# Optimization experiments

Measured on AMD Instinct MI355X. Metric: run time of the kernel, lower is better.

Reference implementation:

```python
import jax, jax.numpy as jnp
import numpy as np

B, D, K = 32768, 256, 4096
BETA = 0.25

def setup_inputs() -> dict:
    key = jax.random.key(0)
    k1, k2 = jax.random.split(key)
    z_e = jax.random.normal(k1, (B, D), dtype=jnp.float32)
    # matches nn.Embedding init: uniform(-1/K, 1/K)
    codebook_weight = jax.random.uniform(k2, (K, D), dtype=jnp.float32,
                                         minval=-1.0 / K, maxval=1.0 / K)
    return {"z_e": z_e, "codebook_weight": codebook_weight}

def reference(z_e, codebook_weight):
    # squared L2 distances [B, K] via expansion: ||z||^2 + ||w||^2 - 2 z.w
    distances = (jnp.sum(z_e ** 2, axis=1, keepdims=True)
                 + jnp.sum(codebook_weight ** 2, axis=1)
                 - 2.0 * z_e @ codebook_weight.T)
    indices = jnp.argmin(distances, axis=1)            # [B] int
    z_q = codebook_weight[indices]                     # [B, D] gather

    codebook_loss = jnp.mean((z_q - jax.lax.stop_gradient(z_e)) ** 2)
    commitment_loss = jnp.mean((z_e - jax.lax.stop_gradient(z_q)) ** 2)
    quant_loss = codebook_loss + BETA * commitment_loss

    # straight-through estimator
    z_q_st = z_e + jax.lax.stop_gradient(z_q - z_e)

    # perplexity: avoid materializing [B, K] one-hot; bincount == one_hot.mean
    counts = jnp.bincount(indices, length=K).astype(jnp.float32)
    avg_probs = counts / z_e.shape[0]
    perplexity = jnp.exp(-jnp.sum(avg_probs * jnp.log(avg_probs + 1e-10)))

    return z_q_st, indices, quant_loss, perplexity
```

## Files before the change

kernel.cpp:

```cpp
#include <hip/hip_runtime.h>
#include <math.h>

constexpr int NROWS = 32768;
constexpr int DIMC  = 256;
constexpr int KC    = 4096;

typedef __attribute__((ext_vector_type(8))) short short8;
typedef __attribute__((ext_vector_type(4))) float f32x4;

#define AS1 __attribute__((address_space(1)))
#define AS3 __attribute__((address_space(3)))

#define WINQ 420u

__device__ __forceinline__ unsigned short f2bf(float x) {
  unsigned u = __float_as_uint(x);
  return (unsigned short)((u + 0x7fffu + ((u >> 16) & 1u)) >> 16);
}

__global__ __launch_bounds__(256)
void vq_prep(const float* __restrict__ Z, const float* __restrict__ W,
             unsigned short* __restrict__ Zh, unsigned short* __restrict__ Wh) {
  const bool isW = blockIdx.x >= 1024;
  const int bid  = isW ? ((int)blockIdx.x - 1024) : (int)blockIdx.x;
  const float* X = isW ? W : Z;
  unsigned short* out = isW ? Wh : Zh;
  const int blk = bid >> 2;
  const int kb0 = (bid & 3) * 2;
  const int t = threadIdx.x;

#pragma unroll
  for (int kk = 0; kk < 2; ++kk) {
    const int kb = kb0 + kk;
#pragma unroll
    for (int gi = 0; gi < 2; ++gi) {
      const int g = t + gi * 256;
      const int r = g >> 2, slot = g & 3;
      const int s8 = slot ^ ((r >> 1) & 3);
      const float* src = X + (size_t)(blk * 128 + r) * DIMC + kb * 32 + s8 * 8;
      short8 vh;
#pragma unroll
      for (int j = 0; j < 8; ++j) vh[j] = (short)f2bf(src[j]);
      *(short8*)(out + ((size_t)blk * 8 + kb) * 4096 + g * 8) = vh;
    }
  }
}

#define DPP_MIN4(v)                                                            \
  {                                                                            \
    unsigned _t;                                                               \
    _t = (unsigned)__builtin_amdgcn_update_dpp((int)(v), (int)(v), 0x121, 0xF, 0xF, false); \
    (v) = min((v), _t);                                                        \
    _t = (unsigned)__builtin_amdgcn_update_dpp((int)(v), (int)(v), 0x122, 0xF, 0xF, false); \
    (v) = min((v), _t);                                                        \
    _t = (unsigned)__builtin_amdgcn_update_dpp((int)(v), (int)(v), 0x124, 0xF, 0xF, false); \
    (v) = min((v), _t);                                                        \
    _t = (unsigned)__builtin_amdgcn_update_dpp((int)(v), (int)(v), 0x128, 0xF, 0xF, false); \
    (v) = min((v), _t);                                                        \
  }

__global__ __launch_bounds__(256, 4)
void vq_mfma(const unsigned short* __restrict__ Zh, const unsigned short* __restrict__ Wh,
             uint2* __restrict__ partial) {
  __shared__ char lds[16384];
  const int t = threadIdx.x, lane = t & 63, w = t >> 6;
  const int rb = blockIdx.x >> 5, cb = blockIdx.x & 31;
  const int q = lane >> 4, ml = lane & 15;
  const int wr = w >> 1, wc = w & 1;

  const unsigned short* bsrc = Wh + (size_t)cb * 32768 + (w >> 1) * 4096
                             + (w & 1) * 2048 + lane * 8;
  char* bdst = lds + (w >> 1) * 8192 + (w & 1) * 4096;

  int aoff[4], boff[4];
#pragma unroll
  for (int i = 0; i < 4; ++i) {
    const int r = wr * 64 + i * 16 + ml;
    aoff[i] = (r * 4 + (q ^ ((r >> 1) & 3))) * 16;
    const int c = wc * 64 + i * 16 + ml;
    boff[i] = (c * 4 + (q ^ ((c >> 1) & 3))) * 16;
  }
  const char* Abase = (const char*)Zh + (size_t)rb * 65536;

  f32x4 acc[4][4];
#pragma unroll
  for (int i = 0; i < 4; ++i)
#pragma unroll
    for (int j = 0; j < 4; ++j) acc[i][j] = (f32x4){0.f, 0.f, 0.f, 0.f};

  for (int kb2 = 0; kb2 < 4; ++kb2) {
    __syncthreads();
#pragma unroll
    for (int i = 0; i < 4; ++i)
      __builtin_amdgcn_global_load_lds((const AS1 void*)(bsrc + kb2 * 8192 + i * 512),
                                       (AS3 void*)(bdst + i * 1024), 16, 0, 0);
    short8 Af[2][4];
#pragma unroll
    for (int sec = 0; sec < 2; ++sec) {
      const int kb = kb2 * 2 + sec;
#pragma unroll
      for (int i = 0; i < 4; ++i)
        Af[sec][i] = *(const short8*)(Abase + (size_t)kb * 8192 + aoff[i]);
    }
    __syncthreads();
#pragma unroll
    for (int sec = 0; sec < 2; ++sec) {
      short8 Bf[4];
#pragma unroll
      for (int i = 0; i < 4; ++i)
        Bf[i] = *(const short8*)(lds + sec * 8192 + boff[i]);
#pragma unroll
      for (int i = 0; i < 4; ++i)
#pragma unroll
        for (int j = 0; j < 4; ++j)
          acc[i][j] = __builtin_amdgcn_mfma_f32_16x16x32_bf16(Af[sec][i], Bf[j], acc[i][j], 0, 0, 0);
    }
  }

  __syncthreads();
  uint2* pk = (uint2*)lds;
  const float SCN = -4194304.0f;

#pragma unroll
  for (int i = 0; i < 4; ++i) {
#pragma unroll
    for (int r = 0; r < 4; ++r) {
      unsigned k[4];
#pragma unroll
      for (int j = 0; j < 4; ++j) {
        const unsigned qv = (unsigned)fmaf(acc[i][j][r], SCN, 524288.0f);
        k[j] = (qv << 7) + (unsigned)(wc * 64 + j * 16 + ml);
      }
      const unsigned m01 = min(k[0], k[1]), x01 = max(k[0], k[1]);
      const unsigned m23 = min(k[2], k[3]), x23 = max(k[2], k[3]);
      const unsigned k1l = min(m01, m23);
      const unsigned k2l = min(max(m01, m23), min(x01, x23));
      unsigned m1 = k1l;
      DPP_MIN4(m1)
      unsigned c2 = (k1l == m1) ? k2l : k1l;
      DPP_MIN4(c2)
      if (ml == 0) pk[w * 64 + (i * 16 + q * 4 + r)] = make_uint2(m1, c2);
    }
  }
  __syncthreads();
  if (t < 128) {
    const int wrh = t >> 6, lr = t & 63;
    const uint2 A2 = pk[(wrh * 2 + 0) * 64 + lr];
    const uint2 B2 = pk[(wrh * 2 + 1) * 64 + lr];
    const unsigned k1 = min(A2.x, B2.x);
    const unsigned k2 = min(min(A2.y, B2.y), max(A2.x, B2.x));
    const unsigned g1 = ((k1 >> 7) << 12) | ((unsigned)cb << 7) | (k1 & 127u);
    const unsigned g2 = ((k2 >> 7) << 12) | ((unsigned)cb << 7) | (k2 & 127u);
    const int row = rb * 128 + wrh * 64 + lr;
    partial[(size_t)row * 32 + cb] = make_uint2(g1, g2);
  }
}

__device__ __forceinline__ float exact_d(const float* __restrict__ Z,
                                         const float* __restrict__ W,
                                         int row, int c, float a) {
  const float* z = Z + (size_t)row * DIMC;
  const float* w = W + (size_t)c * DIMC;
  float dot = 0.f;
  for (int d0 = 0; d0 < DIMC; d0 += 4) {
    const float4 zv = *(const float4*)(z + d0);
    const float4 wv = *(const float4*)(w + d0);
    dot = fmaf(zv.x, wv.x, dot);
    dot = fmaf(zv.y, wv.y, dot);
    dot = fmaf(zv.z, wv.z, dot);
    dot = fmaf(zv.w, wv.w, dot);
  }
  return a - 2.0f * dot;
}

__global__ __launch_bounds__(256)
void vq_tailA(const float* __restrict__ Z, const float* __restrict__ W,
              const uint2* __restrict__ partial, int* __restrict__ kbuf) {
  const int lane = threadIdx.x & 63, wv = threadIdx.x >> 6;
  const int row = blockIdx.x * 4 + wv;
  const float INF = 3.4e38f;

  unsigned k1 = 0xFFFFFFFFu, k2 = 0xFFFFFFFFu;
  if (lane < 32) {
    const uint2 p = partial[(size_t)row * 32 + lane];
    k1 = p.x; k2 = p.y;
  }
  unsigned g1 = k1, g2 = k2;
#pragma unroll
  for (int mask = 1; mask < 32; mask <<= 1) {
    const unsigned og1 = (unsigned)__shfl_xor((int)g1, mask);
    const unsigned og2 = (unsigned)__shfl_xor((int)g2, mask);
    const unsigned mx = max(g1, og1);
    g1 = min(g1, og1);
    g2 = min(min(g2, og2), mx);
  }
  g1 = (unsigned)__shfl((int)g1, 0);
  g2 = (unsigned)__shfl((int)g2, 0);

  int k;
  const unsigned q1 = g1 >> 12;
  if ((g2 >> 12) - q1 > WINQ) {
    k = (int)(g1 & 4095u);
  } else {
    const float4 z4 = *(const float4*)(Z + (size_t)row * DIMC + lane * 4);
    double ns = (double)z4.x * z4.x + (double)z4.y * z4.y +
                (double)z4.z * z4.z + (double)z4.w * z4.w;
#pragma unroll
    for (int mask = 1; mask < 64; mask <<= 1) ns += __shfl_xor(ns, mask);
    const float a = (float)ns;

    const bool scan   = (lane < 32) && ((k2 >> 12) <= q1 + WINQ);
    const bool single = (lane < 32) && !scan && ((k1 >> 12) <= q1 + WINQ);
    float bd = INF; int bi = 0x7fffffff;
    if (single) {
      const int c = (int)(k1 & 4095u);
      const float d = exact_d(Z, W, row, c, a);
      if (d < bd || (d == bd && c < bi)) { bd = d; bi = c; }
    }
    unsigned long long msk = __ballot(scan);
    while (msk) {
      const int cbk = __ffsll(msk) - 1; msk &= msk - 1;
#pragma unroll
      for (int h = 0; h < 2; ++h) {
        const int c = cbk * 128 + h * 64 + lane;
        const float d = exact_d(Z, W, row, c, a);
        if (d < bd || (d == bd && c < bi)) { bd = d; bi = c; }
      }
    }
#pragma unroll
    for (int mask = 1; mask < 64; mask <<= 1) {
      const float od = __shfl_xor(bd, mask);
      const int   oi = __shfl_xor(bi, mask);
      if (od < bd || (od == bd && oi < bi)) { bd = od; bi = oi; }
    }
    k = bi;
  }
  if (lane == 0) kbuf[row] = k;
}

__global__ __launch_bounds__(256)
void vq_tailB(const float* __restrict__ Z, const float* __restrict__ W,
              const int* __restrict__ kbuf, float* __restrict__ zq_out,
              float* __restrict__ idx_out, double* __restrict__ lossp,
              int* __restrict__ hist) {
  __shared__ double sh[4];
  const int lane = threadIdx.x & 63, wv = threadIdx.x >> 6;
  const int row = blockIdx.x * 4 + wv;

  const int k = kbuf[row];
  const float4 z4 = *(const float4*)(Z + (size_t)row * DIMC + lane * 4);
  const float4 w4 = *(const float4*)(W + (size_t)k   * DIMC + lane * 4);
  *(float4*)(zq_out + (size_t)row * DIMC + lane * 4) = w4;

  const double dx = (double)w4.x - (double)z4.x;
  const double dy = (double)w4.y - (double)z4.y;
  const double dz = (double)w4.z - (double)z4.z;
  const double dw = (double)w4.w - (double)z4.w;
  double l = dx * dx + dy * dy + dz * dz + dw * dw;
#pragma unroll
  for (int off = 32; off > 0; off >>= 1) l += __shfl_down(l, off);

  if (lane == 0) { sh[wv] = l; idx_out[row] = (float)k; atomicAdd(&hist[k], 1); }
  __syncthreads();
  if (threadIdx.x == 0) lossp[blockIdx.x] = sh[0] + sh[1] + sh[2] + sh[3];
}

__global__ __launch_bounds__(1024)
void vq_final(const double* __restrict__ lossp, const int* __restrict__ hist,
              float* __restrict__ scal) {
  __shared__ double sL[16], sH[16];
  const int t = threadIdx.x, lane = t & 63, wv = t >> 6;
  double L = 0.0, H = 0.0;
  for (int i = t; i < NROWS / 4; i += 1024) L += lossp[i];
  for (int k = t; k < KC; k += 1024) {
    const double p = (double)hist[k] / (double)NROWS;
    H -= p * log(p + 1e-10);
  }
#pragma unroll
  for (int off = 32; off > 0; off >>= 1) {
    L += __shfl_down(L, off);
    H += __shfl_down(H, off);
  }
  if (lane == 0) { sL[wv] = L; sH[wv] = H; }
  __syncthreads();
  if (t == 0) {
    double LT = 0.0, HT = 0.0;
#pragma unroll
    for (int i = 0; i < 16; ++i) { LT += sL[i]; HT += sH[i]; }
    scal[0] = (float)(LT * 1.25 / ((double)NROWS * (double)DIMC));
    scal[1] = (float)exp(HT);
  }
}

extern "C" void kernel_launch(void* const* d_in, const int* in_sizes, int n_in,
                              void* d_out, int out_size, void* d_ws, size_t ws_size,
                              hipStream_t stream) {
  const float* Z = (const float*)d_in[0];
  const float* W = (const float*)d_in[1];
  float* out = (float*)d_out;
  float* zq_out  = out;
  float* idx_out = out + (size_t)NROWS * DIMC;
  float* scal    = idx_out + NROWS;

  char* ws = (char*)d_ws;
  int*    hist       = (int*)(ws + 1024);
  int*    kbuf       = (int*)(ws + 262144);
  double* lossp      = (double*)(ws + 524288);
  uint2*  partial    = (uint2*)(ws + 1048576);
  unsigned short* Zh = (unsigned short*)(ws + 20971520);
  unsigned short* Wh = (unsigned short*)(ws + 37748736);

  hipMemsetAsync(ws, 0, 17408, stream);
  vq_prep<<<1152, 256, 0, stream>>>(Z, W, Zh, Wh);
  vq_mfma<<<8192, 256, 0, stream>>>(Zh, Wh, partial);
  vq_tailA<<<NROWS / 4, 256, 0, stream>>>(Z, W, partial, kbuf);
  vq_tailB<<<NROWS / 4, 256, 0, stream>>>(Z, W, kbuf, zq_out, idx_out, lossp, hist);
  vq_final<<<1, 1024, 0, stream>>>(lossp, hist, scal);
}
```

Before: 230.1 us.

## Load codebook fragments directly from global into registers with double buffering

Drops the LDS staging of codebook tiles (global_load_lds plus two barriers per step). Each wave now loads its A and B fragments straight from global memory into registers, prefetching the next k-block while the MFMAs for the current one run. The aim is to remove the barrier stalls and LDS traffic. In exchange it doubles fragment register use, which forces launch bounds down from 4 to 3 waves per SIMD, and B tiles are now re-read from global or L2 by each wave instead of being shared through LDS.

```diff
diff --git a/kernel.cpp b/kernel.cpp
--- a/kernel.cpp
+++ b/kernel.cpp
@@ -7,9 +7,6 @@
 
 typedef __attribute__((ext_vector_type(8))) short short8;
 typedef __attribute__((ext_vector_type(4))) float f32x4;
-
-#define AS1 __attribute__((address_space(1)))
-#define AS3 __attribute__((address_space(3)))
 
 #define WINQ 420u
 
@@ -59,18 +56,14 @@
     (v) = min((v), _t);                                                        \
   }
 
-__global__ __launch_bounds__(256, 4)
+__global__ __launch_bounds__(256, 3)
 void vq_mfma(const unsigned short* __restrict__ Zh, const unsigned short* __restrict__ Wh,
              uint2* __restrict__ partial) {
-  __shared__ char lds[16384];
+  __shared__ uint2 pk[256];
   const int t = threadIdx.x, lane = t & 63, w = t >> 6;
   const int rb = blockIdx.x >> 5, cb = blockIdx.x & 31;
   const int q = lane >> 4, ml = lane & 15;
   const int wr = w >> 1, wc = w & 1;
-
-  const unsigned short* bsrc = Wh + (size_t)cb * 32768 + (w >> 1) * 4096
-                             + (w & 1) * 2048 + lane * 8;
-  char* bdst = lds + (w >> 1) * 8192 + (w & 1) * 4096;
 
   int aoff[4], boff[4];
 #pragma unroll
@@ -81,6 +74,7 @@
     boff[i] = (c * 4 + (q ^ ((c >> 1) & 3))) * 16;
   }
   const char* Abase = (const char*)Zh + (size_t)rb * 65536;
+  const char* Bbase = (const char*)Wh + (size_t)cb * 65536;
 
   f32x4 acc[4][4];
 #pragma unroll
@@ -88,37 +82,29 @@
 #pragma unroll
     for (int j = 0; j < 4; ++j) acc[i][j] = (f32x4){0.f, 0.f, 0.f, 0.f};
 
-  for (int kb2 = 0; kb2 < 4; ++kb2) {
-    __syncthreads();
+  short8 Af[2][4], Bf[2][4];
+#pragma unroll
+  for (int i = 0; i < 4; ++i) {
+    Af[0][i] = *(const short8*)(Abase + aoff[i]);
+    Bf[0][i] = *(const short8*)(Bbase + boff[i]);
+  }
+#pragma unroll
+  for (int kb = 0; kb < 8; ++kb) {
+    const int cur = kb & 1, nxt = cur ^ 1;
+    if (kb < 7) {
+#pragma unroll
+      for (int i = 0; i < 4; ++i) {
+        Af[nxt][i] = *(const short8*)(Abase + (kb + 1) * 8192 + aoff[i]);
+        Bf[nxt][i] = *(const short8*)(Bbase + (kb + 1) * 8192 + boff[i]);
+      }
+    }
 #pragma unroll
     for (int i = 0; i < 4; ++i)
-      __builtin_amdgcn_global_load_lds((const AS1 void*)(bsrc + kb2 * 8192 + i * 512),
-                                       (AS3 void*)(bdst + i * 1024), 16, 0, 0);
-    short8 Af[2][4];
-#pragma unroll
-    for (int sec = 0; sec < 2; ++sec) {
-      const int kb = kb2 * 2 + sec;
-#pragma unroll
-      for (int i = 0; i < 4; ++i)
-        Af[sec][i] = *(const short8*)(Abase + (size_t)kb * 8192 + aoff[i]);
-    }
-    __syncthreads();
-#pragma unroll
-    for (int sec = 0; sec < 2; ++sec) {
-      short8 Bf[4];
-#pragma unroll
-      for (int i = 0; i < 4; ++i)
-        Bf[i] = *(const short8*)(lds + sec * 8192 + boff[i]);
-#pragma unroll
-      for (int i = 0; i < 4; ++i)
-#pragma unroll
-        for (int j = 0; j < 4; ++j)
-          acc[i][j] = __builtin_amdgcn_mfma_f32_16x16x32_bf16(Af[sec][i], Bf[j], acc[i][j], 0, 0, 0);
-    }
-  }
-
-  __syncthreads();
-  uint2* pk = (uint2*)lds;
+#pragma unroll
+      for (int j = 0; j < 4; ++j)
+        acc[i][j] = __builtin_amdgcn_mfma_f32_16x16x32_bf16(Af[cur][i], Bf[cur][j], acc[i][j], 0, 0, 0);
+  }
+
   const float SCN = -4194304.0f;
 
 #pragma unroll
```

Result: slower. 265.7 us (+15.4%).

## Fuse tail kernels with last-block reduction and fold memset into prep

Applied to the files above, without the earlier changes.

Merges the argmin refinement, gather/loss/histogram and final reduction kernels into one tail kernel, where the last block to finish (found through an atomic counter) computes the loss and perplexity. Zeroing of the counter and histogram moves from a separate memset into block 0 of the prep kernel. The MFMA kernel's block index is also remapped so that consecutive blocks spread across row and column tiles, which changes cache locality. This removes three launches and the kbuf round trip, at the cost of a serialized single-block final reduction and a dependency on fence and atomic ordering.

```diff
diff --git a/kernel.cpp b/kernel.cpp
--- a/kernel.cpp
+++ b/kernel.cpp
@@ -20,14 +20,22 @@
 
 __global__ __launch_bounds__(256)
 void vq_prep(const float* __restrict__ Z, const float* __restrict__ W,
-             unsigned short* __restrict__ Zh, unsigned short* __restrict__ Wh) {
+             unsigned short* __restrict__ Zh, unsigned short* __restrict__ Wh,
+             int* __restrict__ clr) {
+  const int t = threadIdx.x;
+  if (blockIdx.x == 0) {
+#pragma unroll
+    for (int i = 0; i < 17; ++i) {
+      const int idx = t + i * 256;
+      if (idx < 4352) clr[idx] = 0;
+    }
+  }
   const bool isW = blockIdx.x >= 1024;
   const int bid  = isW ? ((int)blockIdx.x - 1024) : (int)blockIdx.x;
   const float* X = isW ? W : Z;
   unsigned short* out = isW ? Wh : Zh;
   const int blk = bid >> 2;
   const int kb0 = (bid & 3) * 2;
-  const int t = threadIdx.x;
 
 #pragma unroll
   for (int kk = 0; kk < 2; ++kk) {
@@ -64,7 +72,9 @@
              uint2* __restrict__ partial) {
   __shared__ char lds[16384];
   const int t = threadIdx.x, lane = t & 63, w = t >> 6;
-  const int rb = blockIdx.x >> 5, cb = blockIdx.x & 31;
+  const int bid = (int)blockIdx.x;
+  const int sbid = ((bid & 7) << 10) + (bid >> 3);
+  const int rb = sbid >> 5, cb = sbid & 31;
   const int q = lane >> 4, ml = lane & 15;
   const int wr = w >> 1, wc = w & 1;
 
@@ -174,8 +184,13 @@
 }
 
 __global__ __launch_bounds__(256)
-void vq_tailA(const float* __restrict__ Z, const float* __restrict__ W,
-              const uint2* __restrict__ partial, int* __restrict__ kbuf) {
+void vq_tail(const float* __restrict__ Z, const float* __restrict__ W,
+             const uint2* __restrict__ partial, float* __restrict__ zq_out,
+             float* __restrict__ idx_out, double* __restrict__ lossp,
+             int* __restrict__ hist, int* __restrict__ cnt,
+             float* __restrict__ scal) {
+  __shared__ double sh[4];
+  __shared__ int s_last;
   const int lane = threadIdx.x & 63, wv = threadIdx.x >> 6;
   const int row = blockIdx.x * 4 + wv;
   const float INF = 3.4e38f;
@@ -197,12 +212,13 @@
   g1 = (unsigned)__shfl((int)g1, 0);
   g2 = (unsigned)__shfl((int)g2, 0);
 
+  const float4 z4 = *(const float4*)(Z + (size_t)row * DIMC + lane * 4);
+
   int k;
   const unsigned q1 = g1 >> 12;
   if ((g2 >> 12) - q1 > WINQ) {
     k = (int)(g1 & 4095u);
   } else {
-    const float4 z4 = *(const float4*)(Z + (size_t)row * DIMC + lane * 4);
     double ns = (double)z4.x * z4.x + (double)z4.y * z4.y +
                 (double)z4.z * z4.z + (double)z4.w * z4.w;
 #pragma unroll
@@ -235,21 +251,8 @@
     }
     k = bi;
   }
-  if (lane == 0) kbuf[row] = k;
-}
-
-__global__ __launch_bounds__(256)
-void vq_tailB(const float* __restrict__ Z, const float* __restrict__ W,
-              const int* __restrict__ kbuf, float* __restrict__ zq_out,
-              float* __restrict__ idx_out, double* __restrict__ lossp,
-              int* __restrict__ hist) {
-  __shared__ double sh[4];
-  const int lane = threadIdx.x & 63, wv = threadIdx.x >> 6;
-  const int row = blockIdx.x * 4 + wv;
-
-  const int k = kbuf[row];
-  const float4 z4 = *(const float4*)(Z + (size_t)row * DIMC + lane * 4);
-  const float4 w4 = *(const float4*)(W + (size_t)k   * DIMC + lane * 4);
+
+  const float4 w4 = *(const float4*)(W + (size_t)k * DIMC + lane * 4);
   *(float4*)(zq_out + (size_t)row * DIMC + lane * 4) = w4;
 
   const double dx = (double)w4.x - (double)z4.x;
@@ -262,18 +265,26 @@
 
   if (lane == 0) { sh[wv] = l; idx_out[row] = (float)k; atomicAdd(&hist[k], 1); }
   __syncthreads();
-  if (threadIdx.x == 0) lossp[blockIdx.x] = sh[0] + sh[1] + sh[2] + sh[3];
-}
-
-__global__ __launch_bounds__(1024)
-void vq_final(const double* __restrict__ lossp, const int* __restrict__ hist,
-              float* __restrict__ scal) {
-  __shared__ double sL[16], sH[16];
-  const int t = threadIdx.x, lane = t & 63, wv = t >> 6;
+  if (threadIdx.x == 0) {
+    lossp[blockIdx.x] = sh[0] + sh[1] + sh[2] + sh[3];
+    __threadfence();
+    s_last = (atomicAdd(cnt, 1) == (int)gridDim.x - 1) ? 1 : 0;
+  }
+  __syncthreads();
+  if (!s_last) return;
+
+  __shared__ double sL[4], sH[4];
   double L = 0.0, H = 0.0;
-  for (int i = t; i < NROWS / 4; i += 1024) L += lossp[i];
-  for (int k = t; k < KC; k += 1024) {
-    const double p = (double)hist[k] / (double)NROWS;
+  for (int i = threadIdx.x; i < NROWS / 4; i += 256) {
+    const unsigned long long u =
+        __hip_atomic_load((const unsigned long long*)&lossp[i],
+                          __ATOMIC_RELAXED, __HIP_MEMORY_SCOPE_AGENT);
+    L += __longlong_as_double((long long)u);
+  }
+  for (int i = threadIdx.x; i < KC; i += 256) {
+    const int h = __hip_atomic_load(&hist[i], __ATOMIC_RELAXED,
+                                    __HIP_MEMORY_SCOPE_AGENT);
+    const double p = (double)h / (double)NROWS;
     H -= p * log(p + 1e-10);
   }
 #pragma unroll
@@ -283,10 +294,9 @@
   }
   if (lane == 0) { sL[wv] = L; sH[wv] = H; }
   __syncthreads();
-  if (t == 0) {
-    double LT = 0.0, HT = 0.0;
-#pragma unroll
-    for (int i = 0; i < 16; ++i) { LT += sL[i]; HT += sH[i]; }
+  if (threadIdx.x == 0) {
+    const double LT = sL[0] + sL[1] + sL[2] + sL[3];
+    const double HT = sH[0] + sH[1] + sH[2] + sH[3];
     scal[0] = (float)(LT * 1.25 / ((double)NROWS * (double)DIMC));
     scal[1] = (float)exp(HT);
   }
@@ -303,17 +313,15 @@
   float* scal    = idx_out + NROWS;
 
   char* ws = (char*)d_ws;
+  int*    cnt        = (int*)ws;
   int*    hist       = (int*)(ws + 1024);
-  int*    kbuf       = (int*)(ws + 262144);
   double* lossp      = (double*)(ws + 524288);
   uint2*  partial    = (uint2*)(ws + 1048576);
   unsigned short* Zh = (unsigned short*)(ws + 20971520);
   unsigned short* Wh = (unsigned short*)(ws + 37748736);
 
-  hipMemsetAsync(ws, 0, 17408, stream);
-  vq_prep<<<1152, 256, 0, stream>>>(Z, W, Zh, Wh);
+  vq_prep<<<1152, 256, 0, stream>>>(Z, W, Zh, Wh, (int*)ws);
   vq_mfma<<<8192, 256, 0, stream>>>(Zh, Wh, partial);
-  vq_tailA<<<NROWS / 4, 256, 0, stream>>>(Z, W, partial, kbuf);
-  vq_tailB<<<NROWS / 4, 256, 0, stream>>>(Z, W, kbuf, zq_out, idx_out, lossp, hist);
-  vq_final<<<1, 1024, 0, stream>>>(lossp, hist, scal);
-}
+  vq_tail<<<NROWS / 4, 256, 0, stream>>>(Z, W, partial, zq_out, idx_out,
+                                         lossp, hist, cnt, scal);
+}
```

New measurement: 453.4 us. 1.97x slower.

## Fuse tail kernels, fold memset into prep, remap GEMM block order

Applied to the files above, without the earlier changes.

Merges the two tail kernels into one so the chosen index stays in registers and the row of Z is loaded once, removing a launch and the kbuf round trip. The workspace memset is replaced by block 0 of the prep kernel clearing the histogram area, which drops one more launch. The MFMA grid index is permuted so that consecutive blocks are spread across row/column tiles, likely to improve cache locality or XCD distribution. Risks: the clearing is only correct because later kernels run after prep on the same stream.

```diff
diff --git a/kernel.cpp b/kernel.cpp
--- a/kernel.cpp
+++ b/kernel.cpp
@@ -20,14 +20,22 @@
 
 __global__ __launch_bounds__(256)
 void vq_prep(const float* __restrict__ Z, const float* __restrict__ W,
-             unsigned short* __restrict__ Zh, unsigned short* __restrict__ Wh) {
+             unsigned short* __restrict__ Zh, unsigned short* __restrict__ Wh,
+             int* __restrict__ clr) {
+  const int t = threadIdx.x;
+  if (blockIdx.x == 0) {
+#pragma unroll
+    for (int i = 0; i < 17; ++i) {
+      const int idx = t + i * 256;
+      if (idx < 4352) clr[idx] = 0;
+    }
+  }
   const bool isW = blockIdx.x >= 1024;
   const int bid  = isW ? ((int)blockIdx.x - 1024) : (int)blockIdx.x;
   const float* X = isW ? W : Z;
   unsigned short* out = isW ? Wh : Zh;
   const int blk = bid >> 2;
   const int kb0 = (bid & 3) * 2;
-  const int t = threadIdx.x;
 
 #pragma unroll
   for (int kk = 0; kk < 2; ++kk) {
@@ -64,7 +72,9 @@
              uint2* __restrict__ partial) {
   __shared__ char lds[16384];
   const int t = threadIdx.x, lane = t & 63, w = t >> 6;
-  const int rb = blockIdx.x >> 5, cb = blockIdx.x & 31;
+  const int bid = (int)blockIdx.x;
+  const int sbid = ((bid & 7) << 10) + (bid >> 3);
+  const int rb = sbid >> 5, cb = sbid & 31;
   const int q = lane >> 4, ml = lane & 15;
   const int wr = w >> 1, wc = w & 1;
 
@@ -174,8 +184,11 @@
 }
 
 __global__ __launch_bounds__(256)
-void vq_tailA(const float* __restrict__ Z, const float* __restrict__ W,
-              const uint2* __restrict__ partial, int* __restrict__ kbuf) {
+void vq_tail(const float* __restrict__ Z, const float* __restrict__ W,
+             const uint2* __restrict__ partial, float* __restrict__ zq_out,
+             float* __restrict__ idx_out, double* __restrict__ lossp,
+             int* __restrict__ hist) {
+  __shared__ double sh[4];
   const int lane = threadIdx.x & 63, wv = threadIdx.x >> 6;
   const int row = blockIdx.x * 4 + wv;
   const float INF = 3.4e38f;
@@ -197,12 +210,13 @@
   g1 = (unsigned)__shfl((int)g1, 0);
   g2 = (unsigned)__shfl((int)g2, 0);
 
+  const float4 z4 = *(const float4*)(Z + (size_t)row * DIMC + lane * 4);
+
   int k;
   const unsigned q1 = g1 >> 12;
   if ((g2 >> 12) - q1 > WINQ) {
     k = (int)(g1 & 4095u);
   } else {
-    const float4 z4 = *(const float4*)(Z + (size_t)row * DIMC + lane * 4);
     double ns = (double)z4.x * z4.x + (double)z4.y * z4.y +
                 (double)z4.z * z4.z + (double)z4.w * z4.w;
 #pragma unroll
@@ -235,21 +249,8 @@
     }
     k = bi;
   }
-  if (lane == 0) kbuf[row] = k;
-}
-
-__global__ __launch_bounds__(256)
-void vq_tailB(const float* __restrict__ Z, const float* __restrict__ W,
-              const int* __restrict__ kbuf, float* __restrict__ zq_out,
-              float* __restrict__ idx_out, double* __restrict__ lossp,
-              int* __restrict__ hist) {
-  __shared__ double sh[4];
-  const int lane = threadIdx.x & 63, wv = threadIdx.x >> 6;
-  const int row = blockIdx.x * 4 + wv;
-
-  const int k = kbuf[row];
-  const float4 z4 = *(const float4*)(Z + (size_t)row * DIMC + lane * 4);
-  const float4 w4 = *(const float4*)(W + (size_t)k   * DIMC + lane * 4);
+
+  const float4 w4 = *(const float4*)(W + (size_t)k * DIMC + lane * 4);
   *(float4*)(zq_out + (size_t)row * DIMC + lane * 4) = w4;
 
   const double dx = (double)w4.x - (double)z4.x;
@@ -304,16 +305,14 @@
 
   char* ws = (char*)d_ws;
   int*    hist       = (int*)(ws + 1024);
-  int*    kbuf       = (int*)(ws + 262144);
   double* lossp      = (double*)(ws + 524288);
   uint2*  partial    = (uint2*)(ws + 1048576);
   unsigned short* Zh = (unsigned short*)(ws + 20971520);
   unsigned short* Wh = (unsigned short*)(ws + 37748736);
 
-  hipMemsetAsync(ws, 0, 17408, stream);
-  vq_prep<<<1152, 256, 0, stream>>>(Z, W, Zh, Wh);
+  vq_prep<<<1152, 256, 0, stream>>>(Z, W, Zh, Wh, (int*)ws);
   vq_mfma<<<8192, 256, 0, stream>>>(Zh, Wh, partial);
-  vq_tailA<<<NROWS / 4, 256, 0, stream>>>(Z, W, partial, kbuf);
-  vq_tailB<<<NROWS / 4, 256, 0, stream>>>(Z, W, kbuf, zq_out, idx_out, lossp, hist);
+  vq_tail<<<NROWS / 4, 256, 0, stream>>>(Z, W, partial, zq_out, idx_out,
+                                         lossp, hist);
   vq_final<<<1, 1024, 0, stream>>>(lossp, hist, scal);
 }
```

Measured after the change: 228.4 us. No clear change (-0.8%).
